# Optimization experiments

Hardware: AMD Instinct MI355X
Metric: run time of the kernel (lower is better)

Reference implementation:

```python
import jax, jax.numpy as jnp
import numpy as np

B, IN_DIM, OUT_DIM, DEGREE = 4096, 1024, 1024, 4
LN_EPS = 1e-5


def setup_inputs() -> dict:
    key = jax.random.key(0)
    k_x, k_c = jax.random.split(key)
    x = jax.random.normal(k_x, (B, IN_DIM), dtype=jnp.float32)
    # xavier_normal_ on tensor of shape (in, out, deg+1): fan_in/fan_out from
    # torch convention: fan_in = out*(deg+1)? torch computes fan_in=size(1)*receptive,
    # for 3D tensor fan_in = shape[1]*shape[2], fan_out = shape[0]*shape[2].
    fan_in = OUT_DIM * (DEGREE + 1)
    fan_out = IN_DIM * (DEGREE + 1)
    std = float(np.sqrt(2.0 / (fan_in + fan_out)))
    cheby_coeffs = jax.random.normal(k_c, (IN_DIM, OUT_DIM, DEGREE + 1), dtype=jnp.float32) * std
    ln_weight = jnp.ones((IN_DIM,), dtype=jnp.float32)
    ln_bias = jnp.zeros((IN_DIM,), dtype=jnp.float32)
    return {"x": x, "cheby_coeffs": cheby_coeffs, "ln_weight": ln_weight, "ln_bias": ln_bias}


def _layer_norm(x, w, b):
    mu = jnp.mean(x, axis=-1, keepdims=True)
    var = jnp.mean(jnp.square(x - mu), axis=-1, keepdims=True)
    return (x - mu) * jax.lax.rsqrt(var + LN_EPS) * w + b


def reference(x, cheby_coeffs, ln_weight, ln_bias):
    h = jnp.tanh(_layer_norm(x, ln_weight, ln_bias))  # [B, I]
    # Chebyshev recurrence T0=1, T1=h, T_{n}=2h*T_{n-1}-T_{n-2}
    cheby = [jnp.ones_like(h), h]
    for _ in range(2, DEGREE + 1):
        cheby.append(2.0 * h * cheby[-1] - cheby[-2])
    stacked = jnp.stack(cheby, axis=-1)  # [B, I, D+1]
    y = jnp.einsum('bid,iod->bo', stacked, cheby_coeffs)
    return jax.nn.silu(y)
```

## Files before the change

kernel.cpp:

```cpp
#include <hip/hip_runtime.h>
#include <cstdint>
#include <cstddef>

#define BATCH 4096
#define IDIM 1024
#define ODIM 1024
#define KDIM 4096

typedef __attribute__((ext_vector_type(4))) int i32x4;
typedef __attribute__((ext_vector_type(16))) int i32x16;

#define CS_INV 1514.7f
#define DEQ_SCALE (6.602e-4f / 127.0f)

__device__ __forceinline__ char q8(float v, float s) {
  int i = __float2int_rn(v * s);
  i = max(-127, min(127, i));
  return (char)i;
}

__device__ __forceinline__ float tanh_fast(float x) {
  float xc = fminf(fmaxf(x, -20.f), 20.f);
  float t = __expf(2.0f * xc);
  return 1.0f - 2.0f / (t + 1.0f);
}

__device__ __forceinline__ void load_lds16(const void* g, void* l) {
  __builtin_amdgcn_global_load_lds(
      (const __attribute__((address_space(1))) void*)g,
      (__attribute__((address_space(3))) void*)l, 16, 0, 0);
}

#define LNBLK 1024

__global__ __launch_bounds__(256) void prep(
    const float* __restrict__ x, const float* __restrict__ lnw,
    const float* __restrict__ lnb, const float* __restrict__ C,
    char* __restrict__ A, char* __restrict__ Bq,
    float* __restrict__ bias_part) {
  int bid = blockIdx.x;
  int t = threadIdx.x;

  if (bid < LNBLK) {
    int lane = t & 63, wv = t >> 6;
    int row = bid * 4 + wv;
    const float* xr = x + (size_t)row * IDIM;

    float4 v[4], w4[4], b4[4];
#pragma unroll
    for (int j = 0; j < 4; j++) {
      int off = j * 64 + lane;
      v[j]  = ((const float4*)xr)[off];
      w4[j] = ((const float4*)lnw)[off];
      b4[j] = ((const float4*)lnb)[off];
    }
    float s = 0.f, s2 = 0.f;
#pragma unroll
    for (int j = 0; j < 4; j++) {
      s  += v[j].x + v[j].y + v[j].z + v[j].w;
      s2 += v[j].x * v[j].x + v[j].y * v[j].y +
            v[j].z * v[j].z + v[j].w * v[j].w;
    }
#pragma unroll
    for (int off = 32; off > 0; off >>= 1) {
      s  += __shfl_xor(s, off);
      s2 += __shfl_xor(s2, off);
    }
    float mean = s * (1.0f / IDIM);
    float var  = s2 * (1.0f / IDIM) - mean * mean;
    float rstd = rsqrtf(var + 1e-5f);

    size_t base = (size_t)row * KDIM;
#pragma unroll
    for (int j = 0; j < 4; j++) {
      float xs[4] = {v[j].x, v[j].y, v[j].z, v[j].w};
      float ws[4] = {w4[j].x, w4[j].y, w4[j].z, w4[j].w};
      float bs[4] = {b4[j].x, b4[j].y, b4[j].z, b4[j].w};
      char q1[4], q2[4], q3[4], q4[4];
#pragma unroll
      for (int k = 0; k < 4; k++) {
        float h  = tanh_fast((xs[k] - mean) * rstd * ws[k] + bs[k]);
        float T2 = 2.0f * h * h - 1.0f;
        float T3 = 2.0f * h * T2 - h;
        float T4 = 2.0f * h * T3 - T2;
        q1[k] = q8(h, 127.f); q2[k] = q8(T2, 127.f);
        q3[k] = q8(T3, 127.f); q4[k] = q8(T4, 127.f);
      }
      int col = j * 256 + lane * 4;
      *(uint32_t*)(A + base + 0 * IDIM + col) = *(uint32_t*)q1;
      *(uint32_t*)(A + base + 1 * IDIM + col) = *(uint32_t*)q2;
      *(uint32_t*)(A + base + 2 * IDIM + col) = *(uint32_t*)q3;
      *(uint32_t*)(A + base + 3 * IDIM + col) = *(uint32_t*)q4;
    }
  } else {
    __shared__ __align__(16) char smq[5 * 64 * 64];
    __shared__ float smf[64 * 64];
    int cb = bid - LNBLK;
    int i0 = (cb & 15) * 64, o0 = (cb >> 4) * 64;
#pragma unroll
    for (int r = 0; r < 20; r++) {
      int idx = r * 256 + t;
      int ii  = idx / 80;
      int c4  = idx - ii * 80;
      const float4 f = *(const float4*)(C + ((size_t)(i0 + ii) * ODIM + o0) * 5 + c4 * 4);
      float vals[4] = {f.x, f.y, f.z, f.w};
#pragma unroll
      for (int j = 0; j < 4; j++) {
        int p  = c4 * 4 + j;
        int oo = p / 5, d = p - oo * 5;
        if (d == 0) smf[oo * 64 + ii] = vals[j];
        else        smq[p * 64 + ((ii + 4 * p) & 63)] = q8(vals[j], CS_INV);
      }
    }
    __syncthreads();
#pragma unroll
    for (int r = 0; r < 16; r++) {
      int idx = r * 256 + t;
      int seg = idx >> 4, l16 = idx & 15;
      int oo = seg >> 2, d2 = seg & 3;
      int p = oo * 5 + d2 + 1;
      char4 u = *(const char4*)&smq[p * 64 + 4 * ((l16 + p) & 15)];
      *(char4*)(Bq + (size_t)(o0 + oo) * KDIM + d2 * IDIM + i0 + l16 * 4) = u;
    }
    if (t < 64) {
      float s = 0.f;
#pragma unroll
      for (int k = 0; k < 64; k++) s += smf[t * 64 + ((k + t) & 63)];
      bias_part[(cb & 15) * ODIM + o0 + t] = s;
    }
  }
}

#define BM 128
#define BN 128
#define BKB 128
#define NIT (KDIM / BKB)
#define BUFB (BM * BKB)

#define WAIT_BAR(N)                                                          \
  do {                                                                       \
    asm volatile("s_waitcnt vmcnt(" #N ")" ::: "memory");                    \
    __builtin_amdgcn_s_barrier();                                            \
  } while (0)

__global__ __launch_bounds__(512, 1) void gemm_fused(
    const char* __restrict__ A,
    const char* __restrict__ Bq,
    const float* __restrict__ bias_part,
    float* __restrict__ out) {
  __shared__ char As[4][BUFB];
  __shared__ char Bs[4][BUFB];
  int t = threadIdx.x;
  int lane = t & 63, w = t >> 6;

  int bid = blockIdx.x;
  int swz = ((bid & 7) << 5) | (bid >> 3);
  int m0 = (swz >> 3) * BM;
  int n0 = (swz & 7) * BN;

  i32x16 acc[2];
#pragma unroll
  for (int i = 0; i < 2; i++)
#pragma unroll
    for (int r = 0; r < 16; r++) acc[i][r] = 0;

  int wm = (w >> 2) * 64;
  int wn = (w & 3) * 32;

  int sr = lane >> 3;
  int sc = ((lane & 7) ^ sr) * 16;
  const char* ag[2]; char* al[2];
  const char* bg[2]; char* bl[2];
#pragma unroll
  for (int q = 0; q < 2; q++) {
    int row = w * 16 + q * 8;
    ag[q] = A  + (size_t)(m0 + row + sr) * KDIM + sc;
    al[q] = &As[0][row * BKB];
    bg[q] = Bq + (size_t)(n0 + row + sr) * KDIM + sc;
    bl[q] = &Bs[0][row * BKB];
  }

  int l31 = lane & 31, hb = lane >> 5, x7 = lane & 7;
  int arow0 = (wm + l31) * BKB;
  int brow0 = (wn + l31) * BKB;

#define ISSUE(buf, kk0)                                                      \
  do {                                                                       \
    int _k = (kk0);                                                          \
    _Pragma("unroll")                                                        \
    for (int q = 0; q < 2; q++) load_lds16(ag[q] + _k, al[q] + (buf) * BUFB); \
    _Pragma("unroll")                                                        \
    for (int q = 0; q < 2; q++) load_lds16(bg[q] + _k, bl[q] + (buf) * BUFB); \
  } while (0)

#define COMPUTE(buf)                                                         \
  do {                                                                       \
    const char* asb = &As[buf][0];                                           \
    const char* bsb = &Bs[buf][0];                                           \
    _Pragma("unroll")                                                        \
    for (int ks = 0; ks < 4; ks++) {                                         \
      int co = ((2 * ks + hb) ^ x7) * 16;                                    \
      i32x4 af[2], bf;                                                       \
      _Pragma("unroll")                                                      \
      for (int i = 0; i < 2; i++)                                            \
        af[i]  = *(const i32x4*)(asb + arow0 + i * 32 * BKB + co);           \
      bf = *(const i32x4*)(bsb + brow0 + co);                                \
      __builtin_amdgcn_s_setprio(1);                                         \
      _Pragma("unroll")                                                      \
      for (int i = 0; i < 2; i++)                                            \
        acc[i] = __builtin_amdgcn_mfma_i32_32x32x32_i8(                      \
            af[i], bf, acc[i], 0, 0, 0);                                     \
      __builtin_amdgcn_s_setprio(0);                                         \
    }                                                                        \
  } while (0)

  ISSUE(0, 0);
  ISSUE(1, 1 * BKB);
  ISSUE(2, 2 * BKB);

#pragma unroll 1
  for (int jj = 0; jj < 28; jj += 4) {
    WAIT_BAR(8); ISSUE(3, (jj + 3) * BKB); COMPUTE(0);
    WAIT_BAR(8); ISSUE(0, (jj + 4) * BKB); COMPUTE(1);
    WAIT_BAR(8); ISSUE(1, (jj + 5) * BKB); COMPUTE(2);
    WAIT_BAR(8); ISSUE(2, (jj + 6) * BKB); COMPUTE(3);
  }
  WAIT_BAR(8); ISSUE(3, 31 * BKB); COMPUTE(0);
  WAIT_BAR(8); COMPUTE(1);
  WAIT_BAR(4); COMPUTE(2);
  WAIT_BAR(0); COMPUTE(3);

  {
    int col = n0 + wn + l31;
    float bcol = 0.f;
#pragma unroll
    for (int ib = 0; ib < 16; ib++) bcol += bias_part[ib * ODIM + col];
#pragma unroll
    for (int ii = 0; ii < 2; ii++) {
      int rbase = m0 + wm + ii * 32 + 4 * hb;
#pragma unroll
      for (int reg = 0; reg < 16; reg++) {
        int row = rbase + (reg & 3) + 8 * (reg >> 2);
        float y = (float)acc[ii][reg] * DEQ_SCALE + bcol;
        out[(size_t)row * ODIM + col] = y / (1.0f + __expf(-y));
      }
    }
  }
}

extern "C" void kernel_launch(void* const* d_in, const int* in_sizes, int n_in,
                              void* d_out, int out_size, void* d_ws, size_t ws_size,
                              hipStream_t stream) {
  const float* x    = (const float*)d_in[0];
  const float* coef = (const float*)d_in[1];
  const float* lnw  = (const float*)d_in[2];
  const float* lnb  = (const float*)d_in[3];
  float* out = (float*)d_out;

  char* ws = (char*)d_ws;
  char* A    = ws;
  char* Bq   = ws + (size_t)BATCH * KDIM;
  float* bias_part = (float*)(Bq + (size_t)ODIM * KDIM);

  prep<<<LNBLK + 256, 256, 0, stream>>>(x, lnw, lnb, coef, A, Bq, bias_part);
  gemm_fused<<<dim3(256), 512, 0, stream>>>(A, Bq, bias_part, out);
}
```

Baseline: 126.8 us.

## Shrink GEMM tile to 64x128 with 256-thread blocks and double buffering

Halves the GEMM M-tile to 64 rows and uses 256-thread blocks, launching 512 blocks with launch bounds allowing three blocks per CU. The hand-tuned four-stage LDS pipeline with partial vmcnt waits is replaced by simple double buffering with __syncthreads, and the s_setprio hints are dropped. The intent is to hide memory latency through more resident blocks rather than deep explicit prefetch. In exchange, each block reuses loaded data over a smaller tile, so global and LDS traffic per MFMA rises, and the pipeline has less lookahead.

```diff
diff --git a/kernel.cpp b/kernel.cpp
--- a/kernel.cpp
+++ b/kernel.cpp
@@ -131,30 +131,25 @@
   }
 }
 
-#define BM 128
+#define BM 64
 #define BN 128
 #define BKB 128
 #define NIT (KDIM / BKB)
-#define BUFB (BM * BKB)
-
-#define WAIT_BAR(N)                                                          \
-  do {                                                                       \
-    asm volatile("s_waitcnt vmcnt(" #N ")" ::: "memory");                    \
-    __builtin_amdgcn_s_barrier();                                            \
-  } while (0)
-
-__global__ __launch_bounds__(512, 1) void gemm_fused(
+#define ABUF (BM * BKB)
+#define BBUF (BN * BKB)
+
+__global__ __launch_bounds__(256, 3) void gemm_fused(
     const char* __restrict__ A,
     const char* __restrict__ Bq,
     const float* __restrict__ bias_part,
     float* __restrict__ out) {
-  __shared__ char As[4][BUFB];
-  __shared__ char Bs[4][BUFB];
+  __shared__ char As[2][ABUF];
+  __shared__ char Bs[2][BBUF];
   int t = threadIdx.x;
   int lane = t & 63, w = t >> 6;
 
   int bid = blockIdx.x;
-  int swz = ((bid & 7) << 5) | (bid >> 3);
+  int swz = ((bid & 7) << 6) | (bid >> 3);
   int m0 = (swz >> 3) * BM;
   int n0 = (swz & 7) * BN;
 
@@ -164,33 +159,35 @@
 #pragma unroll
     for (int r = 0; r < 16; r++) acc[i][r] = 0;
 
-  int wm = (w >> 2) * 64;
-  int wn = (w & 3) * 32;
+  int wn = w * 32;
 
   int sr = lane >> 3;
   int sc = ((lane & 7) ^ sr) * 16;
   const char* ag[2]; char* al[2];
-  const char* bg[2]; char* bl[2];
+  const char* bg[4]; char* bl[4];
 #pragma unroll
   for (int q = 0; q < 2; q++) {
     int row = w * 16 + q * 8;
-    ag[q] = A  + (size_t)(m0 + row + sr) * KDIM + sc;
+    ag[q] = A + (size_t)(m0 + row + sr) * KDIM + sc;
     al[q] = &As[0][row * BKB];
+  }
+#pragma unroll
+  for (int q = 0; q < 4; q++) {
+    int row = w * 32 + q * 8;
     bg[q] = Bq + (size_t)(n0 + row + sr) * KDIM + sc;
     bl[q] = &Bs[0][row * BKB];
   }
 
   int l31 = lane & 31, hb = lane >> 5, x7 = lane & 7;
-  int arow0 = (wm + l31) * BKB;
   int brow0 = (wn + l31) * BKB;
 
 #define ISSUE(buf, kk0)                                                      \
   do {                                                                       \
     int _k = (kk0);                                                          \
     _Pragma("unroll")                                                        \
-    for (int q = 0; q < 2; q++) load_lds16(ag[q] + _k, al[q] + (buf) * BUFB); \
+    for (int q = 0; q < 2; q++) load_lds16(ag[q] + _k, al[q] + (buf) * ABUF); \
     _Pragma("unroll")                                                        \
-    for (int q = 0; q < 2; q++) load_lds16(bg[q] + _k, bl[q] + (buf) * BUFB); \
+    for (int q = 0; q < 4; q++) load_lds16(bg[q] + _k, bl[q] + (buf) * BBUF); \
   } while (0)
 
 #define COMPUTE(buf)                                                         \
@@ -203,32 +200,25 @@
       i32x4 af[2], bf;                                                       \
       _Pragma("unroll")                                                      \
       for (int i = 0; i < 2; i++)                                            \
-        af[i]  = *(const i32x4*)(asb + arow0 + i * 32 * BKB + co);           \
+        af[i]  = *(const i32x4*)(asb + (l31 + i * 32) * BKB + co);           \
       bf = *(const i32x4*)(bsb + brow0 + co);                                \
-      __builtin_amdgcn_s_setprio(1);                                         \
       _Pragma("unroll")                                                      \
       for (int i = 0; i < 2; i++)                                            \
         acc[i] = __builtin_amdgcn_mfma_i32_32x32x32_i8(                      \
             af[i], bf, acc[i], 0, 0, 0);                                     \
-      __builtin_amdgcn_s_setprio(0);                                         \
     }                                                                        \
   } while (0)
 
   ISSUE(0, 0);
-  ISSUE(1, 1 * BKB);
-  ISSUE(2, 2 * BKB);
-
 #pragma unroll 1
-  for (int jj = 0; jj < 28; jj += 4) {
-    WAIT_BAR(8); ISSUE(3, (jj + 3) * BKB); COMPUTE(0);
-    WAIT_BAR(8); ISSUE(0, (jj + 4) * BKB); COMPUTE(1);
-    WAIT_BAR(8); ISSUE(1, (jj + 5) * BKB); COMPUTE(2);
-    WAIT_BAR(8); ISSUE(2, (jj + 6) * BKB); COMPUTE(3);
-  }
-  WAIT_BAR(8); ISSUE(3, 31 * BKB); COMPUTE(0);
-  WAIT_BAR(8); COMPUTE(1);
-  WAIT_BAR(4); COMPUTE(2);
-  WAIT_BAR(0); COMPUTE(3);
+  for (int it = 0; it < NIT; it += 2) {
+    __syncthreads();
+    if (it + 1 < NIT) ISSUE(1, (it + 1) * BKB);
+    COMPUTE(0);
+    __syncthreads();
+    if (it + 2 < NIT) ISSUE(0, (it + 2) * BKB);
+    COMPUTE(1);
+  }
 
   {
     int col = n0 + wn + l31;
@@ -237,7 +227,7 @@
     for (int ib = 0; ib < 16; ib++) bcol += bias_part[ib * ODIM + col];
 #pragma unroll
     for (int ii = 0; ii < 2; ii++) {
-      int rbase = m0 + wm + ii * 32 + 4 * hb;
+      int rbase = m0 + ii * 32 + 4 * hb;
 #pragma unroll
       for (int reg = 0; reg < 16; reg++) {
         int row = rbase + (reg & 3) + 8 * (reg >> 2);
@@ -263,5 +253,5 @@
   float* bias_part = (float*)(Bq + (size_t)ODIM * KDIM);
 
   prep<<<LNBLK + 256, 256, 0, stream>>>(x, lnw, lnb, coef, A, Bq, bias_part);
-  gemm_fused<<<dim3(256), 512, 0, stream>>>(A, Bq, bias_part, out);
-}
+  gemm_fused<<<dim3(512), 256, 0, stream>>>(A, Bq, bias_part, out);
+}
```

New measurement: 129.4 us. +2.0%, slower.

## Split K across two warp groups with 64x64 warp tiles and LDS reduction

Applied to the files above, without the earlier changes.

Reorganizes the int8 GEMM so the 8 waves form two groups that each process alternating K-chunks, with every wave computing a 64x64 tile (2x2 MFMA blocks) instead of 64x32. This raises MFMA work per LDS fragment load. The two groups' partial accumulators are summed through LDS before the epilogue. The pipeline changes from a 3-deep prefetch with partial vmcnt waits to a double buffer per group with full vmcnt(0) waits, which may expose more load latency and adds a reduction step.

```diff
diff --git a/kernel.cpp b/kernel.cpp
--- a/kernel.cpp
+++ b/kernel.cpp
@@ -134,12 +134,11 @@
 #define BM 128
 #define BN 128
 #define BKB 128
-#define NIT (KDIM / BKB)
 #define BUFB (BM * BKB)
 
-#define WAIT_BAR(N)                                                          \
+#define WAIT_BAR0                                                            \
   do {                                                                       \
-    asm volatile("s_waitcnt vmcnt(" #N ")" ::: "memory");                    \
+    asm volatile("s_waitcnt vmcnt(0)" ::: "memory");                         \
     __builtin_amdgcn_s_barrier();                                            \
   } while (0)
 
@@ -152,97 +151,120 @@
   __shared__ char Bs[4][BUFB];
   int t = threadIdx.x;
   int lane = t & 63, w = t >> 6;
+  int wg = w & 3, g = w >> 2;
 
   int bid = blockIdx.x;
   int swz = ((bid & 7) << 5) | (bid >> 3);
   int m0 = (swz >> 3) * BM;
   int n0 = (swz & 7) * BN;
 
-  i32x16 acc[2];
+  i32x16 acc[2][2];
 #pragma unroll
   for (int i = 0; i < 2; i++)
 #pragma unroll
-    for (int r = 0; r < 16; r++) acc[i][r] = 0;
-
-  int wm = (w >> 2) * 64;
-  int wn = (w & 3) * 32;
+    for (int j = 0; j < 2; j++)
+#pragma unroll
+      for (int r = 0; r < 16; r++) acc[i][j][r] = 0;
+
+  int wm = (wg >> 1) * 64;
+  int wn = (wg & 1) * 64;
 
   int sr = lane >> 3;
   int sc = ((lane & 7) ^ sr) * 16;
-  const char* ag[2]; char* al[2];
-  const char* bg[2]; char* bl[2];
-#pragma unroll
-  for (int q = 0; q < 2; q++) {
-    int row = w * 16 + q * 8;
+  const char* ag[4]; char* al[4];
+  const char* bg[4]; char* bl[4];
+#pragma unroll
+  for (int q = 0; q < 4; q++) {
+    int row = wg * 32 + q * 8;
     ag[q] = A  + (size_t)(m0 + row + sr) * KDIM + sc;
-    al[q] = &As[0][row * BKB];
+    al[q] = &As[0][row * BKB] + g * BUFB;
     bg[q] = Bq + (size_t)(n0 + row + sr) * KDIM + sc;
-    bl[q] = &Bs[0][row * BKB];
+    bl[q] = &Bs[0][row * BKB] + g * BUFB;
   }
 
   int l31 = lane & 31, hb = lane >> 5, x7 = lane & 7;
   int arow0 = (wm + l31) * BKB;
   int brow0 = (wn + l31) * BKB;
-
-#define ISSUE(buf, kk0)                                                      \
+  const char* asb0 = &As[0][0] + g * BUFB;
+  const char* bsb0 = &Bs[0][0] + g * BUFB;
+
+#define ISSUE(bofs, cj)                                                      \
   do {                                                                       \
-    int _k = (kk0);                                                          \
+    int _k = (cj) * BKB;                                                     \
     _Pragma("unroll")                                                        \
-    for (int q = 0; q < 2; q++) load_lds16(ag[q] + _k, al[q] + (buf) * BUFB); \
+    for (int q = 0; q < 4; q++) load_lds16(ag[q] + _k, al[q] + (bofs));      \
     _Pragma("unroll")                                                        \
-    for (int q = 0; q < 2; q++) load_lds16(bg[q] + _k, bl[q] + (buf) * BUFB); \
+    for (int q = 0; q < 4; q++) load_lds16(bg[q] + _k, bl[q] + (bofs));      \
   } while (0)
 
-#define COMPUTE(buf)                                                         \
+#define COMPUTE(bofs)                                                        \
   do {                                                                       \
-    const char* asb = &As[buf][0];                                           \
-    const char* bsb = &Bs[buf][0];                                           \
+    const char* asb = asb0 + (bofs);                                         \
+    const char* bsb = bsb0 + (bofs);                                         \
     _Pragma("unroll")                                                        \
     for (int ks = 0; ks < 4; ks++) {                                         \
       int co = ((2 * ks + hb) ^ x7) * 16;                                    \
-      i32x4 af[2], bf;                                                       \
+      i32x4 af[2], bf[2];                                                    \
       _Pragma("unroll")                                                      \
       for (int i = 0; i < 2; i++)                                            \
-        af[i]  = *(const i32x4*)(asb + arow0 + i * 32 * BKB + co);           \
-      bf = *(const i32x4*)(bsb + brow0 + co);                                \
+        af[i] = *(const i32x4*)(asb + arow0 + i * 32 * BKB + co);            \
+      _Pragma("unroll")                                                      \
+      for (int j = 0; j < 2; j++)                                            \
+        bf[j] = *(const i32x4*)(bsb + brow0 + j * 32 * BKB + co);            \
       __builtin_amdgcn_s_setprio(1);                                         \
       _Pragma("unroll")                                                      \
       for (int i = 0; i < 2; i++)                                            \
-        acc[i] = __builtin_amdgcn_mfma_i32_32x32x32_i8(                      \
-            af[i], bf, acc[i], 0, 0, 0);                                     \
+        _Pragma("unroll")                                                    \
+        for (int j = 0; j < 2; j++)                                          \
+          acc[i][j] = __builtin_amdgcn_mfma_i32_32x32x32_i8(                 \
+              af[i], bf[j], acc[i][j], 0, 0, 0);                             \
       __builtin_amdgcn_s_setprio(0);                                         \
     }                                                                        \
   } while (0)
 
-  ISSUE(0, 0);
-  ISSUE(1, 1 * BKB);
-  ISSUE(2, 2 * BKB);
+  ISSUE(0, g);
 
 #pragma unroll 1
-  for (int jj = 0; jj < 28; jj += 4) {
-    WAIT_BAR(8); ISSUE(3, (jj + 3) * BKB); COMPUTE(0);
-    WAIT_BAR(8); ISSUE(0, (jj + 4) * BKB); COMPUTE(1);
-    WAIT_BAR(8); ISSUE(1, (jj + 5) * BKB); COMPUTE(2);
-    WAIT_BAR(8); ISSUE(2, (jj + 6) * BKB); COMPUTE(3);
-  }
-  WAIT_BAR(8); ISSUE(3, 31 * BKB); COMPUTE(0);
-  WAIT_BAR(8); COMPUTE(1);
-  WAIT_BAR(4); COMPUTE(2);
-  WAIT_BAR(0); COMPUTE(3);
-
-  {
-    int col = n0 + wn + l31;
-    float bcol = 0.f;
-#pragma unroll
-    for (int ib = 0; ib < 16; ib++) bcol += bias_part[ib * ODIM + col];
-#pragma unroll
-    for (int ii = 0; ii < 2; ii++) {
-      int rbase = m0 + wm + ii * 32 + 4 * hb;
-#pragma unroll
-      for (int reg = 0; reg < 16; reg++) {
-        int row = rbase + (reg & 3) + 8 * (reg >> 2);
-        float y = (float)acc[ii][reg] * DEQ_SCALE + bcol;
-        out[(size_t)row * ODIM + col] = y / (1.0f + __expf(-y));
+  for (int s = 0; s < 16; s += 2) {
+    WAIT_BAR0;
+    if (s + 1 < 16) ISSUE(2 * BUFB, 2 * s + 2 + g);
+    COMPUTE(0);
+    WAIT_BAR0;
+    if (s + 2 < 16) ISSUE(0, 2 * s + 4 + g);
+    COMPUTE(2 * BUFB);
+  }
+
+  __syncthreads();
+  int* xch = (int*)&As[0][0];
+  if (g == 1) {
+    int* p = xch + wg * 4096 + lane;
+#pragma unroll
+    for (int ii = 0; ii < 2; ii++)
+#pragma unroll
+      for (int jj = 0; jj < 2; jj++)
+#pragma unroll
+        for (int r = 0; r < 16; r++)
+          p[((ii * 2 + jj) * 16 + r) * 64] = acc[ii][jj][r];
+  }
+  __syncthreads();
+  if (g == 0) {
+    const int* p = xch + wg * 4096 + lane;
+#pragma unroll
+    for (int jj = 0; jj < 2; jj++) {
+      int col = n0 + wn + jj * 32 + l31;
+      float bcol = 0.f;
+#pragma unroll
+      for (int ib = 0; ib < 16; ib++) bcol += bias_part[ib * ODIM + col];
+#pragma unroll
+      for (int ii = 0; ii < 2; ii++) {
+        int rbase = m0 + wm + ii * 32 + 4 * hb;
+#pragma unroll
+        for (int reg = 0; reg < 16; reg++) {
+          int row = rbase + (reg & 3) + 8 * (reg >> 2);
+          int sum = acc[ii][jj][reg] + p[((ii * 2 + jj) * 16 + reg) * 64];
+          float y = (float)sum * DEQ_SCALE + bcol;
+          out[(size_t)row * ODIM + col] = y / (1.0f + __expf(-y));
+        }
       }
     }
   }
```

After: 122.8 us, median of 2. 3.2% less time.
